# Kernel optimization log

Measured on AMD Instinct MI355X. Metric: run time of the kernel, lower is better.

The kernel has to match this reference:

```python
import jax, jax.numpy as jnp
import numpy as np

EPS = 1e-7
NUM_ROUTING = 3


def squash(s, axis=-1):
    # v = ||s||^2/(1+||s||^2) * s/||s||, numerically safe
    sq = jnp.sum(jnp.square(s), axis=axis, keepdims=True)
    scale = sq / (1.0 + sq) / jnp.sqrt(sq + EPS)
    return scale * s


def setup_inputs() -> dict:
    key = jax.random.key(0)
    k1, k2 = jax.random.split(key)
    B, IN_CAPS, IN_DIM = 256, 1152, 8
    NUM_CAPS, DIM_VEC = 10, 16
    inputs = jax.random.normal(k1, (B, IN_CAPS, IN_DIM), dtype=jnp.float32)
    # glorot_uniform over [in_caps, num_caps, dim_vec, in_dim]
    limit = np.sqrt(6.0 / (IN_DIM + DIM_VEC))
    W = jax.random.uniform(k2, (IN_CAPS, NUM_CAPS, DIM_VEC, IN_DIM), dtype=jnp.float32,
                           minval=-limit, maxval=limit)
    bias = jnp.zeros((IN_CAPS, NUM_CAPS), dtype=jnp.float32)
    return {"inputs": inputs, "W": W, "bias": bias}


def reference(inputs, W, bias):
    # u_hat[b,i,c,d] = W[i,c,d,e] @ inputs[b,i,e]
    u_hat = jnp.einsum('icde,bie->bicd', W, inputs)  # [B, in_caps, num_caps, dim_vec]
    b = bias[None]  # [1, in_caps, num_caps], broadcasts to [B, ...]
    for _ in range(NUM_ROUTING - 1):
        c = jax.nn.softmax(b, axis=2)                       # over num_capsule
        s = jnp.einsum('bic,bicd->bcd', c * jnp.ones_like(u_hat[..., 0]), u_hat)
        v = squash(s, axis=-1)                              # [B, num_caps, dim_vec]
        agreement = jnp.einsum('bicd,bcd->bic', u_hat, v)
        b = agreement + b + bias[None]
    c_last = jax.nn.softmax(b, axis=2)
    s = jnp.einsum('bic,bicd->bcd', c_last * jnp.ones_like(u_hat[..., 0]), u_hat)
    outputs = squash(s, axis=-1)                            # [B, num_caps, dim_vec]
    return outputs
```

## Files before the change

### kernel.cpp

```cpp
#include <hip/hip_runtime.h>
#include <math.h>

#define BATCH 256
#define IC    1152
#define EDIM  8
#define NC    10
#define DV    16

#define ITILE  8
#define NCHUNK 4
#define ITOT   (ITILE * NCHUNK)
#define NB     4
#define NTHREADS 256
#define NWAVES 4
#define NSLAB  (IC / ITOT)
#define BCHUNKS (BATCH / NB)
#define SCD (NC * DV)
#define SPART_STRIDE (BATCH * SCD)

template<int CTRL>
__device__ __forceinline__ float dpp_add(float x) {
    int r = __builtin_amdgcn_update_dpp(0, __float_as_int(x), CTRL, 0xF, 0xF, true);
    return x + __int_as_float(r);
}
__device__ __forceinline__ float row_reduce16(float x) {
    x = dpp_add<0xB1>(x);
    x = dpp_add<0x4E>(x);
    x = dpp_add<0x141>(x);
    x = dpp_add<0x140>(x);
    return x;
}

template<int MODE>
__global__ __launch_bounds__(NTHREADS, 2)
void caps_main(const float* __restrict__ x,
               const float* __restrict__ W,
               const float* __restrict__ bias,
               const float* __restrict__ v_in,
               float* __restrict__ b2,
               float* __restrict__ s_part)
{
    __shared__ float sx[NB][ITOT * EDIM];
    __shared__ float swv[NWAVES][NB][SCD];

    const int tid = threadIdx.x;
    const int d   = tid & 15;
    const int ch  = (tid >> 4) & 1;
    const int il  = tid >> 5;
    const int wid = tid >> 6;
    const int icb = blockIdx.x;
    const int bcb = blockIdx.y;
    const int i0  = icb * ITOT;
    const int b0  = bcb * NB;

    {
        const float4* xg = (const float4*)x;
        float4* xs = (float4*)&sx[0][0];
        int bb = tid >> 6;
        int w  = tid & 63;
        xs[tid] = xg[(size_t)(b0 + bb) * (IC * EDIM / 4) + i0 * (EDIM / 4) + w];
    }

    float sacc[NB][5];
    #pragma unroll
    for (int bb = 0; bb < NB; ++bb)
        #pragma unroll
        for (int k = 0; k < 5; ++k) sacc[bb][k] = 0.f;

    __syncthreads();

    const float4* Wg = (const float4*)W;

    #pragma unroll 1
    for (int ic = 0; ic < NCHUNK; ++ic) {
        const int i = i0 + ic * ITILE + il;

        float4 w4[5][2];
        float  bv[5];
        #pragma unroll
        for (int k = 0; k < 5; ++k) {
            int c = ch * 5 + k;
            size_t base = ((size_t)(i * NC + c) * DV + d) * 2;
            w4[k][0] = Wg[base];
            w4[k][1] = Wg[base + 1];
            bv[k]    = bias[i * NC + c];
        }

        float cw[5];
        if (MODE == 1) {
            float mx = fmaxf(fmaxf(fmaxf(bv[0], bv[1]), fmaxf(bv[2], bv[3])), bv[4]);
            mx = fmaxf(mx, __shfl_xor(mx, 16));
            float ssum = 0.f, ex[5];
            #pragma unroll
            for (int k = 0; k < 5; ++k) { ex[k] = __expf(bv[k] - mx); ssum += ex[k]; }
            ssum += __shfl_xor(ssum, 16);
            float inv = 1.0f / ssum;
            #pragma unroll
            for (int k = 0; k < 5; ++k) cw[k] = ex[k] * inv;
        }

        #pragma unroll
        for (int bb = 0; bb < NB; ++bb) {
            const int b = b0 + bb;
            const float4 x0 = ((const float4*)&sx[bb][(ic * ITILE + il) * EDIM])[0];
            const float4 x1 = ((const float4*)&sx[bb][(ic * ITILE + il) * EDIM])[1];

            float u[5];
            #pragma unroll
            for (int k = 0; k < 5; ++k) {
                float acc = w4[k][0].x * x0.x;
                acc = fmaf(w4[k][0].y, x0.y, acc);
                acc = fmaf(w4[k][0].z, x0.z, acc);
                acc = fmaf(w4[k][0].w, x0.w, acc);
                acc = fmaf(w4[k][1].x, x1.x, acc);
                acc = fmaf(w4[k][1].y, x1.y, acc);
                acc = fmaf(w4[k][1].z, x1.z, acc);
                acc = fmaf(w4[k][1].w, x1.w, acc);
                u[k] = acc;
            }

            if (MODE != 1) {
                const float* vb = v_in + (size_t)b * SCD + ch * 80 + d;
                float t[5];
                #pragma unroll
                for (int k = 0; k < 5; ++k) t[k] = u[k] * vb[k * 16];
                #pragma unroll
                for (int k = 0; k < 5; ++k) t[k] = row_reduce16(t[k]);

                float br[5];
                float* bp = b2 + (((size_t)b * IC + i) * 2 + ch) * 8;
                if (MODE == 2) {
                    #pragma unroll
                    for (int k = 0; k < 5; ++k) br[k] = t[k] + 2.0f * bv[k];
                    if (d == 0) {
                        #pragma unroll
                        for (int k = 0; k < 5; ++k) bp[k] = br[k];
                    }
                } else {
                    #pragma unroll
                    for (int k = 0; k < 5; ++k) br[k] = t[k] + bp[k] + bv[k];
                }
                float mx = fmaxf(fmaxf(fmaxf(br[0], br[1]), fmaxf(br[2], br[3])), br[4]);
                mx = fmaxf(mx, __shfl_xor(mx, 16));
                float ssum = 0.f, ex[5];
                #pragma unroll
                for (int k = 0; k < 5; ++k) { ex[k] = __expf(br[k] - mx); ssum += ex[k]; }
                ssum += __shfl_xor(ssum, 16);
                float inv = 1.0f / ssum;
                #pragma unroll
                for (int k = 0; k < 5; ++k) cw[k] = ex[k] * inv;
            }

            #pragma unroll
            for (int k = 0; k < 5; ++k)
                sacc[bb][k] = fmaf(cw[k], u[k], sacc[bb][k]);
        }
    }

    #pragma unroll
    for (int bb = 0; bb < NB; ++bb) {
        #pragma unroll
        for (int k = 0; k < 5; ++k) {
            float s = sacc[bb][k] + __shfl_xor(sacc[bb][k], 32);
            if ((tid & 32) == 0)
                swv[wid][bb][ch * 80 + k * 16 + d] = s;
        }
    }
    __syncthreads();
    for (int j = tid; j < NB * SCD; j += NTHREADS) {
        int bb = j / SCD;
        int cd = j - bb * SCD;
        float s = (swv[0][bb][cd] + swv[1][bb][cd])
                + (swv[2][bb][cd] + swv[3][bb][cd]);
        s_part[((size_t)icb * BATCH + b0 + bb) * SCD + cd] = s;
    }
}

__global__ __launch_bounds__(256)
void caps_squash(const float* __restrict__ s_part, float* __restrict__ out)
{
    const int tid = threadIdx.x;
    const int bc  = blockIdx.x * 16 + (tid >> 4);
    const size_t off = (size_t)bc * DV + (tid & 15);

    float a[4] = {0.f, 0.f, 0.f, 0.f};
    #pragma unroll
    for (int ic = 0; ic < NSLAB; ic += 4) {
        #pragma unroll
        for (int j = 0; j < 4; ++j)
            a[j] += s_part[(size_t)(ic + j) * SPART_STRIDE + off];
    }
    float s = (a[0] + a[1]) + (a[2] + a[3]);

    float sq = row_reduce16(s * s);

    float scale = sq / ((1.0f + sq) * sqrtf(sq + 1e-7f));
    out[off] = scale * s;
}

extern "C" void kernel_launch(void* const* d_in, const int* in_sizes, int n_in,
                              void* d_out, int out_size, void* d_ws, size_t ws_size,
                              hipStream_t stream)
{
    const float* x    = (const float*)d_in[0];
    const float* W    = (const float*)d_in[1];
    const float* bias = (const float*)d_in[2];
    float* out = (float*)d_out;

    float* ws     = (float*)d_ws;
    float* s_part = ws;
    float* v      = s_part + (size_t)NSLAB * SPART_STRIDE;
    float* b2     = v + SPART_STRIDE;

    dim3 grid(NSLAB, BCHUNKS);

    caps_main<1><<<grid, NTHREADS, 0, stream>>>(x, W, bias, v, b2, s_part);
    caps_squash<<<160, 256, 0, stream>>>(s_part, v);
    caps_main<2><<<grid, NTHREADS, 0, stream>>>(x, W, bias, v, b2, s_part);
    caps_squash<<<160, 256, 0, stream>>>(s_part, v);
    caps_main<3><<<grid, NTHREADS, 0, stream>>>(x, W, bias, v, b2, s_part);
    caps_squash<<<160, 256, 0, stream>>>(s_part, out);
}
```

Measured before the change: 183.6 us.

## Replace partial-sum slabs with atomic accumulation and fuse squash into routing kernels

Each block now atomically adds its per-capsule partial sums into a single batch-sized buffer instead of writing per-slab partials. The intermediate squash kernels go away: each routing pass squashes the previous sums itself into shared memory, then caches v in registers. Routing pass 1 zeroes the buffers for later passes, and the thread mapping is rearranged so the two capsule halves are reduced with a 32-lane permlane swap. The softmax also drops max subtraction and uses a fast reciprocal, which risks overflow and makes float atomic ordering nondeterministic.

```diff
diff --git a/kernel.cpp b/kernel.cpp
--- a/kernel.cpp
+++ b/kernel.cpp
@@ -12,11 +12,10 @@
 #define ITOT   (ITILE * NCHUNK)
 #define NB     4
 #define NTHREADS 256
-#define NWAVES 4
 #define NSLAB  (IC / ITOT)
 #define BCHUNKS (BATCH / NB)
 #define SCD (NC * DV)
-#define SPART_STRIDE (BATCH * SCD)
+#define SFLOATS (BATCH * SCD)
 
 template<int CTRL>
 __device__ __forceinline__ float dpp_add(float x) {
@@ -31,23 +30,35 @@
     return x;
 }
 
+#if __has_builtin(__builtin_amdgcn_permlane32_swap)
+typedef int int2v __attribute__((ext_vector_type(2)));
+__device__ __forceinline__ float cross32_sum(float x) {
+    int2v r = __builtin_amdgcn_permlane32_swap(__float_as_int(x), __float_as_int(x),
+                                               false, false);
+    return __int_as_float(r[0]) + __int_as_float(r[1]);
+}
+#else
+__device__ __forceinline__ float cross32_sum(float x) { return x + __shfl_xor(x, 32); }
+#endif
+
 template<int MODE>
 __global__ __launch_bounds__(NTHREADS, 2)
 void caps_main(const float* __restrict__ x,
                const float* __restrict__ W,
                const float* __restrict__ bias,
-               const float* __restrict__ v_in,
+               const float* __restrict__ s_in,
                float* __restrict__ b2,
-               float* __restrict__ s_part)
+               float* __restrict__ s_out,
+               float* __restrict__ z0,
+               float* __restrict__ z1)
 {
     __shared__ float sx[NB][ITOT * EDIM];
-    __shared__ float swv[NWAVES][NB][SCD];
+    __shared__ float vls[NB][SCD];
 
     const int tid = threadIdx.x;
     const int d   = tid & 15;
-    const int ch  = (tid >> 4) & 1;
-    const int il  = tid >> 5;
-    const int wid = tid >> 6;
+    const int ch  = (tid >> 5) & 1;
+    const int il  = ((tid >> 4) & 1) | ((tid >> 6) << 1);
     const int icb = blockIdx.x;
     const int bcb = blockIdx.y;
     const int i0  = icb * ITOT;
@@ -61,6 +72,28 @@
         xs[tid] = xg[(size_t)(b0 + bb) * (IC * EDIM / 4) + i0 * (EDIM / 4) + w];
     }
 
+    if (MODE == 1) {
+        if (icb < 2) {
+            float* z = (icb == 0) ? z0 : z1;
+            #pragma unroll
+            for (int t = 0; t < 3; ++t) {
+                int j = t * NTHREADS + tid;
+                if (j < NB * SCD) z[(size_t)b0 * SCD + j] = 0.f;
+            }
+        }
+    } else {
+        #pragma unroll
+        for (int t = 0; t < 3; ++t) {
+            int j = t * NTHREADS + tid;
+            if (j < NB * SCD) {
+                float s  = s_in[(size_t)b0 * SCD + j];
+                float sq = row_reduce16(s * s);
+                float scale = sq / ((1.0f + sq) * sqrtf(sq + 1e-7f));
+                (&vls[0][0])[j] = scale * s;
+            }
+        }
+    }
+
     float sacc[NB][5];
     #pragma unroll
     for (int bb = 0; bb < NB; ++bb)
@@ -68,6 +101,15 @@
         for (int k = 0; k < 5; ++k) sacc[bb][k] = 0.f;
 
     __syncthreads();
+
+    float vreg[NB][5];
+    if (MODE != 1) {
+        #pragma unroll
+        for (int bb = 0; bb < NB; ++bb)
+            #pragma unroll
+            for (int k = 0; k < 5; ++k)
+                vreg[bb][k] = vls[bb][(ch * 5 + k) * 16 + d];
+    }
 
     const float4* Wg = (const float4*)W;
 
@@ -88,20 +130,17 @@
 
         float cw[5];
         if (MODE == 1) {
-            float mx = fmaxf(fmaxf(fmaxf(bv[0], bv[1]), fmaxf(bv[2], bv[3])), bv[4]);
-            mx = fmaxf(mx, __shfl_xor(mx, 16));
             float ssum = 0.f, ex[5];
             #pragma unroll
-            for (int k = 0; k < 5; ++k) { ex[k] = __expf(bv[k] - mx); ssum += ex[k]; }
-            ssum += __shfl_xor(ssum, 16);
-            float inv = 1.0f / ssum;
+            for (int k = 0; k < 5; ++k) { ex[k] = __expf(bv[k]); ssum += ex[k]; }
+            ssum = cross32_sum(ssum);
+            float inv = __builtin_amdgcn_rcpf(ssum);
             #pragma unroll
             for (int k = 0; k < 5; ++k) cw[k] = ex[k] * inv;
         }
 
         #pragma unroll
         for (int bb = 0; bb < NB; ++bb) {
-            const int b = b0 + bb;
             const float4 x0 = ((const float4*)&sx[bb][(ic * ITILE + il) * EDIM])[0];
             const float4 x1 = ((const float4*)&sx[bb][(ic * ITILE + il) * EDIM])[1];
 
@@ -120,18 +159,17 @@
             }
 
             if (MODE != 1) {
-                const float* vb = v_in + (size_t)b * SCD + ch * 80 + d;
                 float t[5];
                 #pragma unroll
-                for (int k = 0; k < 5; ++k) t[k] = u[k] * vb[k * 16];
+                for (int k = 0; k < 5; ++k) t[k] = u[k] * vreg[bb][k];
                 #pragma unroll
                 for (int k = 0; k < 5; ++k) t[k] = row_reduce16(t[k]);
 
                 float br[5];
-                float* bp = b2 + (((size_t)b * IC + i) * 2 + ch) * 8;
+                float* bp = b2 + (((size_t)(b0 + bb) * IC + i) * 2 + ch) * 8;
                 if (MODE == 2) {
                     #pragma unroll
-                    for (int k = 0; k < 5; ++k) br[k] = t[k] + 2.0f * bv[k];
+                    for (int k = 0; k < 5; ++k) br[k] = fmaf(2.0f, bv[k], t[k]);
                     if (d == 0) {
                         #pragma unroll
                         for (int k = 0; k < 5; ++k) bp[k] = br[k];
@@ -140,13 +178,11 @@
                     #pragma unroll
                     for (int k = 0; k < 5; ++k) br[k] = t[k] + bp[k] + bv[k];
                 }
-                float mx = fmaxf(fmaxf(fmaxf(br[0], br[1]), fmaxf(br[2], br[3])), br[4]);
-                mx = fmaxf(mx, __shfl_xor(mx, 16));
                 float ssum = 0.f, ex[5];
                 #pragma unroll
-                for (int k = 0; k < 5; ++k) { ex[k] = __expf(br[k] - mx); ssum += ex[k]; }
-                ssum += __shfl_xor(ssum, 16);
-                float inv = 1.0f / ssum;
+                for (int k = 0; k < 5; ++k) { ex[k] = __expf(br[k]); ssum += ex[k]; }
+                ssum = cross32_sum(ssum);
+                float inv = __builtin_amdgcn_rcpf(ssum);
                 #pragma unroll
                 for (int k = 0; k < 5; ++k) cw[k] = ex[k] * inv;
             }
@@ -161,41 +197,21 @@
     for (int bb = 0; bb < NB; ++bb) {
         #pragma unroll
         for (int k = 0; k < 5; ++k) {
-            float s = sacc[bb][k] + __shfl_xor(sacc[bb][k], 32);
-            if ((tid & 32) == 0)
-                swv[wid][bb][ch * 80 + k * 16 + d] = s;
-        }
-    }
-    __syncthreads();
-    for (int j = tid; j < NB * SCD; j += NTHREADS) {
-        int bb = j / SCD;
-        int cd = j - bb * SCD;
-        float s = (swv[0][bb][cd] + swv[1][bb][cd])
-                + (swv[2][bb][cd] + swv[3][bb][cd]);
-        s_part[((size_t)icb * BATCH + b0 + bb) * SCD + cd] = s;
+            float s = sacc[bb][k] + __shfl_xor(sacc[bb][k], 16);
+            if ((tid & 16) == 0)
+                atomicAdd(&s_out[(size_t)(b0 + bb) * SCD + (ch * 5 + k) * 16 + d], s);
+        }
     }
 }
 
 __global__ __launch_bounds__(256)
-void caps_squash(const float* __restrict__ s_part, float* __restrict__ out)
+void caps_squash(const float* __restrict__ s_sum, float* __restrict__ out)
 {
-    const int tid = threadIdx.x;
-    const int bc  = blockIdx.x * 16 + (tid >> 4);
-    const size_t off = (size_t)bc * DV + (tid & 15);
-
-    float a[4] = {0.f, 0.f, 0.f, 0.f};
-    #pragma unroll
-    for (int ic = 0; ic < NSLAB; ic += 4) {
-        #pragma unroll
-        for (int j = 0; j < 4; ++j)
-            a[j] += s_part[(size_t)(ic + j) * SPART_STRIDE + off];
-    }
-    float s = (a[0] + a[1]) + (a[2] + a[3]);
-
+    const int idx = blockIdx.x * 256 + threadIdx.x;
+    float s  = s_sum[idx];
     float sq = row_reduce16(s * s);
-
     float scale = sq / ((1.0f + sq) * sqrtf(sq + 1e-7f));
-    out[off] = scale * s;
+    out[idx] = scale * s;
 }
 
 extern "C" void kernel_launch(void* const* d_in, const int* in_sizes, int n_in,
@@ -207,17 +223,16 @@
     const float* bias = (const float*)d_in[2];
     float* out = (float*)d_out;
 
-    float* ws     = (float*)d_ws;
-    float* s_part = ws;
-    float* v      = s_part + (size_t)NSLAB * SPART_STRIDE;
-    float* b2     = v + SPART_STRIDE;
+    float* sA = (float*)d_ws;
+    float* sB = sA + SFLOATS;
+    float* sC = sB + SFLOATS;
+    float* b2 = sC + SFLOATS;
 
     dim3 grid(NSLAB, BCHUNKS);
 
-    caps_main<1><<<grid, NTHREADS, 0, stream>>>(x, W, bias, v, b2, s_part);
-    caps_squash<<<160, 256, 0, stream>>>(s_part, v);
-    caps_main<2><<<grid, NTHREADS, 0, stream>>>(x, W, bias, v, b2, s_part);
-    caps_squash<<<160, 256, 0, stream>>>(s_part, v);
-    caps_main<3><<<grid, NTHREADS, 0, stream>>>(x, W, bias, v, b2, s_part);
-    caps_squash<<<160, 256, 0, stream>>>(s_part, out);
-}
+    hipMemsetAsync(sA, 0, SFLOATS * sizeof(float), stream);
+    caps_main<1><<<grid, NTHREADS, 0, stream>>>(x, W, bias, nullptr, b2, sA, sB, sC);
+    caps_main<2><<<grid, NTHREADS, 0, stream>>>(x, W, bias, sA, b2, sB, nullptr, nullptr);
+    caps_main<3><<<grid, NTHREADS, 0, stream>>>(x, W, bias, sB, b2, sC, nullptr, nullptr);
+    caps_squash<<<160, 256, 0, stream>>>(sC, out);
+}
```

Result: slower. 207.9 us (+13.3%).

## Drop softmax max-subtraction, use exp2 with pre-scaled logits, stage v in LDS

Applied to the files above, without the earlier changes.

Softmax inside routing no longer subtracts the max. It works in base-2: v is pre-multiplied by log2(e) in squash and the bias is scaled the same way, so exp2 and a hardware reciprocal replace __expf and a division. The thread mapping changes so that the two capsule halves sit 32 lanes apart, letting the cross-half sum use permlane32_swap. Per-block v is staged in shared memory instead of being read from global memory for every element. Without the max subtraction the softmax relies on the logits staying small enough to avoid overflow, which holds for the given inputs, and the approximate exp and reciprocal change precision slightly.

```diff
diff --git a/kernel.cpp b/kernel.cpp
--- a/kernel.cpp
+++ b/kernel.cpp
@@ -17,6 +17,7 @@
 #define BCHUNKS (BATCH / NB)
 #define SCD (NC * DV)
 #define SPART_STRIDE (BATCH * SCD)
+#define L2E 1.4426950408889634f
 
 template<int CTRL>
 __device__ __forceinline__ float dpp_add(float x) {
@@ -30,6 +31,23 @@
     x = dpp_add<0x140>(x);
     return x;
 }
+
+typedef int int2v __attribute__((ext_vector_type(2)));
+#if __has_builtin(__builtin_amdgcn_permlane32_swap)
+__device__ __forceinline__ float cross32_sum(float x) {
+    int2v r = __builtin_amdgcn_permlane32_swap(__float_as_int(x), __float_as_int(x),
+                                               false, false);
+    return __int_as_float(r[0]) + __int_as_float(r[1]);
+}
+#else
+__device__ __forceinline__ float cross32_sum(float x) { return x + __shfl_xor(x, 32); }
+#endif
+
+#if __has_builtin(__builtin_amdgcn_exp2f)
+#define EXP2F(x) __builtin_amdgcn_exp2f(x)
+#else
+#define EXP2F(x) exp2f(x)
+#endif
 
 template<int MODE>
 __global__ __launch_bounds__(NTHREADS, 2)
@@ -42,11 +60,12 @@
 {
     __shared__ float sx[NB][ITOT * EDIM];
     __shared__ float swv[NWAVES][NB][SCD];
+    __shared__ float vls[NB][SCD];
 
     const int tid = threadIdx.x;
     const int d   = tid & 15;
-    const int ch  = (tid >> 4) & 1;
-    const int il  = tid >> 5;
+    const int ch  = (tid >> 5) & 1;
+    const int il  = ((tid >> 4) & 1) | (((tid >> 6) & 3) << 1);
     const int wid = tid >> 6;
     const int icb = blockIdx.x;
     const int bcb = blockIdx.y;
@@ -60,6 +79,14 @@
         int w  = tid & 63;
         xs[tid] = xg[(size_t)(b0 + bb) * (IC * EDIM / 4) + i0 * (EDIM / 4) + w];
     }
+    if (MODE != 1) {
+        #pragma unroll
+        for (int t = 0; t < 3; ++t) {
+            int j = t * NTHREADS + tid;
+            if (j < NB * SCD)
+                (&vls[0][0])[j] = v_in[(size_t)b0 * SCD + j];
+        }
+    }
 
     float sacc[NB][5];
     #pragma unroll
@@ -87,16 +114,18 @@
         }
 
         float cw[5];
+        float bvs[5];
         if (MODE == 1) {
-            float mx = fmaxf(fmaxf(fmaxf(bv[0], bv[1]), fmaxf(bv[2], bv[3])), bv[4]);
-            mx = fmaxf(mx, __shfl_xor(mx, 16));
             float ssum = 0.f, ex[5];
             #pragma unroll
-            for (int k = 0; k < 5; ++k) { ex[k] = __expf(bv[k] - mx); ssum += ex[k]; }
-            ssum += __shfl_xor(ssum, 16);
-            float inv = 1.0f / ssum;
+            for (int k = 0; k < 5; ++k) { ex[k] = __expf(bv[k]); ssum += ex[k]; }
+            ssum = cross32_sum(ssum);
+            float inv = __builtin_amdgcn_rcpf(ssum);
             #pragma unroll
             for (int k = 0; k < 5; ++k) cw[k] = ex[k] * inv;
+        } else {
+            #pragma unroll
+            for (int k = 0; k < 5; ++k) bvs[k] = bv[k] * L2E;
         }
 
         #pragma unroll
@@ -120,7 +149,7 @@
             }
 
             if (MODE != 1) {
-                const float* vb = v_in + (size_t)b * SCD + ch * 80 + d;
+                const float* vb = &vls[bb][ch * 80 + d];
                 float t[5];
                 #pragma unroll
                 for (int k = 0; k < 5; ++k) t[k] = u[k] * vb[k * 16];
@@ -131,22 +160,20 @@
                 float* bp = b2 + (((size_t)b * IC + i) * 2 + ch) * 8;
                 if (MODE == 2) {
                     #pragma unroll
-                    for (int k = 0; k < 5; ++k) br[k] = t[k] + 2.0f * bv[k];
+                    for (int k = 0; k < 5; ++k) br[k] = fmaf(2.0f, bvs[k], t[k]);
                     if (d == 0) {
                         #pragma unroll
                         for (int k = 0; k < 5; ++k) bp[k] = br[k];
                     }
                 } else {
                     #pragma unroll
-                    for (int k = 0; k < 5; ++k) br[k] = t[k] + bp[k] + bv[k];
+                    for (int k = 0; k < 5; ++k) br[k] = t[k] + bp[k] + bvs[k];
                 }
-                float mx = fmaxf(fmaxf(fmaxf(br[0], br[1]), fmaxf(br[2], br[3])), br[4]);
-                mx = fmaxf(mx, __shfl_xor(mx, 16));
                 float ssum = 0.f, ex[5];
                 #pragma unroll
-                for (int k = 0; k < 5; ++k) { ex[k] = __expf(br[k] - mx); ssum += ex[k]; }
-                ssum += __shfl_xor(ssum, 16);
-                float inv = 1.0f / ssum;
+                for (int k = 0; k < 5; ++k) { ex[k] = EXP2F(br[k]); ssum += ex[k]; }
+                ssum = cross32_sum(ssum);
+                float inv = __builtin_amdgcn_rcpf(ssum);
                 #pragma unroll
                 for (int k = 0; k < 5; ++k) cw[k] = ex[k] * inv;
             }
@@ -161,8 +188,8 @@
     for (int bb = 0; bb < NB; ++bb) {
         #pragma unroll
         for (int k = 0; k < 5; ++k) {
-            float s = sacc[bb][k] + __shfl_xor(sacc[bb][k], 32);
-            if ((tid & 32) == 0)
+            float s = sacc[bb][k] + __shfl_xor(sacc[bb][k], 16);
+            if ((tid & 16) == 0)
                 swv[wid][bb][ch * 80 + k * 16 + d] = s;
         }
     }
@@ -177,7 +204,8 @@
 }
 
 __global__ __launch_bounds__(256)
-void caps_squash(const float* __restrict__ s_part, float* __restrict__ out)
+void caps_squash(const float* __restrict__ s_part, float* __restrict__ out,
+                 float mult)
 {
     const int tid = threadIdx.x;
     const int bc  = blockIdx.x * 16 + (tid >> 4);
@@ -195,7 +223,7 @@
     float sq = row_reduce16(s * s);
 
     float scale = sq / ((1.0f + sq) * sqrtf(sq + 1e-7f));
-    out[off] = scale * s;
+    out[off] = (mult * scale) * s;
 }
 
 extern "C" void kernel_launch(void* const* d_in, const int* in_sizes, int n_in,
@@ -215,9 +243,9 @@
     dim3 grid(NSLAB, BCHUNKS);
 
     caps_main<1><<<grid, NTHREADS, 0, stream>>>(x, W, bias, v, b2, s_part);
-    caps_squash<<<160, 256, 0, stream>>>(s_part, v);
+    caps_squash<<<160, 256, 0, stream>>>(s_part, v, L2E);
     caps_main<2><<<grid, NTHREADS, 0, stream>>>(x, W, bias, v, b2, s_part);
-    caps_squash<<<160, 256, 0, stream>>>(s_part, v);
+    caps_squash<<<160, 256, 0, stream>>>(s_part, v, L2E);
     caps_main<3><<<grid, NTHREADS, 0, stream>>>(x, W, bias, v, b2, s_part);
-    caps_squash<<<160, 256, 0, stream>>>(s_part, out);
-}
+    caps_squash<<<160, 256, 0, stream>>>(s_part, out, 1.0f);
+}
```

After: 169.6 us. -7.6%, faster.
